# Performance work log

Measured on AMD Instinct MI355X. Metric: run time of the kernel, lower is better.

The kernel has to match this reference:

```python
import jax, jax.numpy as jnp
import numpy as np

D_K = 64  # per-head dim; source hardcodes d_k for the 1/sqrt(d_k) scale


def setup_inputs() -> dict:
    key = jax.random.key(0)
    kq, kk, kv = jax.random.split(key, 3)
    shape = (4, 16, 2048, D_K)  # [B, H, S, d]
    return {
        "q_s": jax.random.normal(kq, shape, dtype=jnp.float32),
        "k_s": jax.random.normal(kk, shape, dtype=jnp.float32),
        "v_s": jax.random.normal(kv, shape, dtype=jnp.float32),
    }


def reference(q_s, k_s, v_s):
    # scores = Q K^T / sqrt(d_k)  -> [B, H, S, S] (full matrix, unfused, as in source)
    scale = 1.0 / jnp.sqrt(jnp.asarray(D_K, dtype=q_s.dtype))
    scores = jnp.einsum("bhqd,bhkd->bhqk", q_s, k_s) * scale
    attn = jax.nn.softmax(scores, axis=-1)
    # out = attn @ V -> [B, H, S, d]
    return jnp.einsum("bhqk,bhkd->bhqd", attn, v_s)
```

## Files before the change

kernel.cpp:

```cpp
#include <hip/hip_runtime.h>
#include <stdint.h>
#include <math.h>

#define S_LEN 2048
#define DIM   64
#define QBLK  64
#define KVBLK 32
#define NKV   (S_LEN / KVBLK)

typedef __attribute__((ext_vector_type(8))) short short8;
typedef __attribute__((ext_vector_type(4))) float f32x4;

static __device__ __forceinline__ unsigned short f2bf(float f) {
    union { float f; uint32_t u; } cv; cv.f = f;
    uint32_t u = cv.u;
    return (unsigned short)((u + 0x7fffu + ((u >> 16) & 1u)) >> 16);
}

static __device__ __forceinline__ void gload16(const void* g, void* l) {
    __builtin_amdgcn_global_load_lds(
        (const __attribute__((address_space(1))) unsigned int*)g,
        (__attribute__((address_space(3))) unsigned int*)l, 16, 0, 0);
}

static __device__ __forceinline__ float vmax3(float a, float b, float c) {
    float d;
    asm("v_max3_f32 %0, %1, %2, %3" : "=v"(d) : "v"(a), "v"(b), "v"(c));
    return d;
}

__global__ void cvt_k(const float* __restrict__ kp, unsigned short* __restrict__ kws) {
    const int idx = blockIdx.x * 256 + threadIdx.x;
    const int c   = idx & 7;
    const int s   = (idx >> 3) & (S_LEN - 1);
    const int bh  = idx >> 14;
    const float* src = kp + ((size_t)bh * S_LEN + s) * DIM + c * 8;
    const f32x4 a = *reinterpret_cast<const f32x4*>(src);
    const f32x4 b = *reinterpret_cast<const f32x4*>(src + 4);
    short8 t;
    t[0] = (short)f2bf(a[0]); t[1] = (short)f2bf(a[1]);
    t[2] = (short)f2bf(a[2]); t[3] = (short)f2bf(a[3]);
    t[4] = (short)f2bf(b[0]); t[5] = (short)f2bf(b[1]);
    t[6] = (short)f2bf(b[2]); t[7] = (short)f2bf(b[3]);
    unsigned short* dst = kws + ((size_t)bh * S_LEN + s) * DIM + (size_t)((c ^ (s & 7)) * 8);
    *reinterpret_cast<short8*>(dst) = t;
}

__global__ void cvt_v(const float* __restrict__ vp, unsigned short* __restrict__ vtws) {
    const int bh = blockIdx.x >> 5;
    const int T  = blockIdx.x & 31;
    const int tid = threadIdx.x;
    __shared__ unsigned short ldsT[DIM][72];

    const int i = tid >> 2;
    const int dbase = (tid & 3) * 16;
    const float* src = vp + ((size_t)bh * S_LEN + T * 64 + i) * DIM + dbase;
#pragma unroll
    for (int q4 = 0; q4 < 4; ++q4) {
        const f32x4 a = *reinterpret_cast<const f32x4*>(src + q4 * 4);
#pragma unroll
        for (int j = 0; j < 4; ++j) ldsT[dbase + q4 * 4 + j][i] = f2bf(a[j]);
    }
    __syncthreads();
#pragma unroll
    for (int hh = 0; hh < 2; ++hh) {
        const int slot = tid + hh * 256;
        const int d = slot >> 3;
        const int h = (slot >> 2) & 1;
        const int c_st = slot & 3;
        const int cl = c_st ^ ((d >> 1) & 3);
        short8 t8;
#pragma unroll
        for (int j = 0; j < 8; ++j) {
            const int p = cl * 8 + j;
            const int kap = ((p & 4) << 2) | ((p & 16) >> 1) | ((p & 8) >> 1) | (p & 3);
            t8[j] = (short)ldsT[d][h * 32 + kap];
        }
        unsigned short* dst = vtws + ((size_t)bh * DIM + d) * S_LEN + T * 64 + h * 32 + c_st * 8;
        *reinterpret_cast<short8*>(dst) = t8;
    }
}

__global__ __launch_bounds__(256, 8)
void attn_fwd(const float* __restrict__ qp, const unsigned short* __restrict__ kws,
              const unsigned short* __restrict__ vtws, float* __restrict__ op) {
    const int lb = (blockIdx.x & 7) * 256 + (blockIdx.x >> 3);
    const int bh = lb >> 5;
    const int qb = lb & 31;
    const int tid  = threadIdx.x;
    const int wave = tid >> 6;
    const int lane = tid & 63;
    const int g = lane >> 4;
    const int r = lane & 15;

    __shared__ unsigned short klds[2][KVBLK * DIM];
    __shared__ unsigned short vlds[2][DIM * 32];

    const float*          qg    = qp   + (size_t)bh * (S_LEN * DIM);
    const unsigned short* kbase = kws  + (size_t)bh * (S_LEN * DIM);
    const unsigned short* vbase = vtws + (size_t)bh * (S_LEN * DIM);
    float*                og    = op   + (size_t)bh * (S_LEN * DIM);

    const float qscale = 0.125f * 1.44269504088896340736f;
    const int q0 = qb * QBLK + wave * 16;
    short8 qfrag[2];
    {
        const float* qrow = qg + (size_t)(q0 + r) * DIM;
#pragma unroll
        for (int ks = 0; ks < 2; ++ks) {
            const f32x4 a = *reinterpret_cast<const f32x4*>(qrow + ks * 32 + 8 * g);
            const f32x4 b = *reinterpret_cast<const f32x4*>(qrow + ks * 32 + 8 * g + 4);
            short8 t;
            t[0] = (short)f2bf(a[0] * qscale); t[1] = (short)f2bf(a[1] * qscale);
            t[2] = (short)f2bf(a[2] * qscale); t[3] = (short)f2bf(a[3] * qscale);
            t[4] = (short)f2bf(b[0] * qscale); t[5] = (short)f2bf(b[1] * qscale);
            t[6] = (short)f2bf(b[2] * qscale); t[7] = (short)f2bf(b[3] * qscale);
            qfrag[ks] = t;
        }
    }

    f32x4 o[4];
#pragma unroll
    for (int nt = 0; nt < 4; ++nt) { f32x4 z = {0.f, 0.f, 0.f, 0.f}; o[nt] = z; }
    float m_run = -INFINITY, l_part = 0.0f;

    const int srow = lane >> 3, schk = lane & 7;
    const int vd = wave * 16 + ((lane >> 2) & 15), vcst = lane & 3;
    auto stage = [&](int t, int buf) {
        gload16(kbase + (size_t)(t * KVBLK + wave * 8 + srow) * DIM + schk * 8,
                &klds[buf][(wave * 8) * DIM]);
        gload16(vbase + (size_t)vd * S_LEN + (t >> 1) * 64 + (t & 1) * 32 + vcst * 8,
                &vlds[buf][wave * 512]);
    };

    int koff[2][2], voff[4];
#pragma unroll
    for (int nt = 0; nt < 2; ++nt)
#pragma unroll
        for (int ks = 0; ks < 2; ++ks)
            koff[nt][ks] = (nt * 16 + r) * DIM + (((ks << 2) | g) ^ (r & 7)) * 8;
#pragma unroll
    for (int nt = 0; nt < 4; ++nt)
        voff[nt] = (nt * 16 + r) * 32 + (g ^ ((r >> 1) & 3)) * 8;

    const f32x4 z4 = {0.f, 0.f, 0.f, 0.f};

    stage(0, 0);
    __syncthreads();
    int cur = 0;

    for (int t = 0; t < NKV; ++t) {
        if (t + 1 < NKV) stage(t + 1, cur ^ 1);

        const unsigned short* kl = &klds[cur][0];
        __builtin_amdgcn_s_setprio(1);
        const short8 kf00 = *reinterpret_cast<const short8*>(kl + koff[0][0]);
        const short8 kf01 = *reinterpret_cast<const short8*>(kl + koff[0][1]);
        const short8 kf10 = *reinterpret_cast<const short8*>(kl + koff[1][0]);
        const short8 kf11 = *reinterpret_cast<const short8*>(kl + koff[1][1]);
        f32x4 st0 = __builtin_amdgcn_mfma_f32_16x16x32_bf16(kf00, qfrag[0], z4, 0, 0, 0);
        f32x4 st1 = __builtin_amdgcn_mfma_f32_16x16x32_bf16(kf10, qfrag[0], z4, 0, 0, 0);
        st0 = __builtin_amdgcn_mfma_f32_16x16x32_bf16(kf01, qfrag[1], st0, 0, 0, 0);
        st1 = __builtin_amdgcn_mfma_f32_16x16x32_bf16(kf11, qfrag[1], st1, 0, 0, 0);
        __builtin_amdgcn_s_setprio(0);

        const float a0 = vmax3(st0[0], st0[1], st0[2]);
        const float a1 = vmax3(st0[3], st1[0], st1[1]);
        const float a2 = fmaxf(st1[2], st1[3]);
        const float lane_mx = vmax3(a0, a1, a2);
        if (__any(lane_mx > m_run + 8.0f)) {
            float mx = fmaxf(lane_mx, __shfl_xor(lane_mx, 16));
            mx = fmaxf(mx, __shfl_xor(mx, 32));
            const float mnew = fmaxf(m_run, mx);
            const float al = __builtin_amdgcn_exp2f(m_run - mnew);
            m_run = mnew;
            l_part *= al;
#pragma unroll
            for (int nt = 0; nt < 4; ++nt) {
                f32x4 sc = o[nt];
                sc[0] *= al; sc[1] *= al; sc[2] *= al; sc[3] *= al;
                o[nt] = sc;
            }
        }
        f32x4 p0, p1;
        p0[0] = __builtin_amdgcn_exp2f(st0[0] - m_run);
        p0[1] = __builtin_amdgcn_exp2f(st0[1] - m_run);
        p0[2] = __builtin_amdgcn_exp2f(st0[2] - m_run);
        p0[3] = __builtin_amdgcn_exp2f(st0[3] - m_run);
        p1[0] = __builtin_amdgcn_exp2f(st1[0] - m_run);
        p1[1] = __builtin_amdgcn_exp2f(st1[1] - m_run);
        p1[2] = __builtin_amdgcn_exp2f(st1[2] - m_run);
        p1[3] = __builtin_amdgcn_exp2f(st1[3] - m_run);
        l_part += ((p0[0] + p0[1]) + (p0[2] + p0[3])) + ((p1[0] + p1[1]) + (p1[2] + p1[3]));

        short8 pfrag;
        {
            union { uint32_t u[4]; short8 v; } fr;
            asm("v_cvt_pk_bf16_f32 %0, %1, %2" : "=v"(fr.u[0]) : "v"(p0[0]), "v"(p0[1]));
            asm("v_cvt_pk_bf16_f32 %0, %1, %2" : "=v"(fr.u[1]) : "v"(p0[2]), "v"(p0[3]));
            asm("v_cvt_pk_bf16_f32 %0, %1, %2" : "=v"(fr.u[2]) : "v"(p1[0]), "v"(p1[1]));
            asm("v_cvt_pk_bf16_f32 %0, %1, %2" : "=v"(fr.u[3]) : "v"(p1[2]), "v"(p1[3]));
            pfrag = fr.v;
        }

        const unsigned short* vl = &vlds[cur][0];
        __builtin_amdgcn_s_setprio(1);
#pragma unroll
        for (int nt = 0; nt < 4; ++nt) {
            const short8 vf = *reinterpret_cast<const short8*>(vl + voff[nt]);
            o[nt] = __builtin_amdgcn_mfma_f32_16x16x32_bf16(vf, pfrag, o[nt], 0, 0, 0);
        }
        __builtin_amdgcn_s_setprio(0);

        __syncthreads();
        cur ^= 1;
    }

    float lfull = l_part;
    lfull += __shfl_xor(lfull, 16);
    lfull += __shfl_xor(lfull, 32);
    const float inv = 1.0f / lfull;
    float* dst = og + (size_t)(q0 + r) * DIM + 4 * g;
#pragma unroll
    for (int nt = 0; nt < 4; ++nt) {
        f32x4 tt = o[nt];
        tt[0] *= inv; tt[1] *= inv; tt[2] *= inv; tt[3] *= inv;
        *reinterpret_cast<f32x4*>(dst + nt * 16) = tt;
    }
}

extern "C" void kernel_launch(void* const* d_in, const int* in_sizes, int n_in,
                              void* d_out, int out_size, void* d_ws, size_t ws_size,
                              hipStream_t stream) {
    const float* q = (const float*)d_in[0];
    const float* k = (const float*)d_in[1];
    const float* v = (const float*)d_in[2];
    float* out = (float*)d_out;
    unsigned short* kws  = (unsigned short*)d_ws;
    unsigned short* vtws = kws + (size_t)64 * S_LEN * DIM;
    cvt_k<<<dim3(64 * S_LEN * 8 / 256), 256, 0, stream>>>(k, kws);
    cvt_v<<<dim3(64 * (S_LEN / 64)), 256, 0, stream>>>(v, vtws);
    attn_fwd<<<dim3(2048), 256, 0, stream>>>(q, kws, vtws, out);
}
```

Measured before the change: 121.3 us.

## Load K/V fragments directly from global memory instead of staging through LDS

Removes the double-buffered LDS staging of K and V tiles, along with the per-iteration block barrier. Each wave now reads its MFMA operand fragments straight from the pre-swizzled bf16 workspaces in global memory. The launch bound drops from 8 to 5 blocks per CU, which gives the compiler more registers to hold in-flight loads. The cost is that all four waves fetch the same K/V data redundantly through the cache hierarchy. There is also no explicit prefetch of the next tile, so load latency is exposed unless the compiler or occupancy hides it.

```diff
diff --git a/kernel.cpp b/kernel.cpp
--- a/kernel.cpp
+++ b/kernel.cpp
@@ -15,12 +15,6 @@
     union { float f; uint32_t u; } cv; cv.f = f;
     uint32_t u = cv.u;
     return (unsigned short)((u + 0x7fffu + ((u >> 16) & 1u)) >> 16);
-}
-
-static __device__ __forceinline__ void gload16(const void* g, void* l) {
-    __builtin_amdgcn_global_load_lds(
-        (const __attribute__((address_space(1))) unsigned int*)g,
-        (__attribute__((address_space(3))) unsigned int*)l, 16, 0, 0);
 }
 
 static __device__ __forceinline__ float vmax3(float a, float b, float c) {
@@ -81,7 +75,7 @@
     }
 }
 
-__global__ __launch_bounds__(256, 8)
+__global__ __launch_bounds__(256, 5)
 void attn_fwd(const float* __restrict__ qp, const unsigned short* __restrict__ kws,
               const unsigned short* __restrict__ vtws, float* __restrict__ op) {
     const int lb = (blockIdx.x & 7) * 256 + (blockIdx.x >> 3);
@@ -93,9 +87,6 @@
     const int g = lane >> 4;
     const int r = lane & 15;
 
-    __shared__ unsigned short klds[2][KVBLK * DIM];
-    __shared__ unsigned short vlds[2][DIM * 32];
-
     const float*          qg    = qp   + (size_t)bh * (S_LEN * DIM);
     const unsigned short* kbase = kws  + (size_t)bh * (S_LEN * DIM);
     const unsigned short* vbase = vtws + (size_t)bh * (S_LEN * DIM);
@@ -124,15 +115,6 @@
     for (int nt = 0; nt < 4; ++nt) { f32x4 z = {0.f, 0.f, 0.f, 0.f}; o[nt] = z; }
     float m_run = -INFINITY, l_part = 0.0f;
 
-    const int srow = lane >> 3, schk = lane & 7;
-    const int vd = wave * 16 + ((lane >> 2) & 15), vcst = lane & 3;
-    auto stage = [&](int t, int buf) {
-        gload16(kbase + (size_t)(t * KVBLK + wave * 8 + srow) * DIM + schk * 8,
-                &klds[buf][(wave * 8) * DIM]);
-        gload16(vbase + (size_t)vd * S_LEN + (t >> 1) * 64 + (t & 1) * 32 + vcst * 8,
-                &vlds[buf][wave * 512]);
-    };
-
     int koff[2][2], voff[4];
 #pragma unroll
     for (int nt = 0; nt < 2; ++nt)
@@ -141,28 +123,29 @@
             koff[nt][ks] = (nt * 16 + r) * DIM + (((ks << 2) | g) ^ (r & 7)) * 8;
 #pragma unroll
     for (int nt = 0; nt < 4; ++nt)
-        voff[nt] = (nt * 16 + r) * 32 + (g ^ ((r >> 1) & 3)) * 8;
+        voff[nt] = (nt * 16 + r) * S_LEN + (g ^ ((r >> 1) & 3)) * 8;
 
     const f32x4 z4 = {0.f, 0.f, 0.f, 0.f};
 
-    stage(0, 0);
-    __syncthreads();
-    int cur = 0;
-
     for (int t = 0; t < NKV; ++t) {
-        if (t + 1 < NKV) stage(t + 1, cur ^ 1);
-
-        const unsigned short* kl = &klds[cur][0];
+        const int kt = t * (KVBLK * DIM);
+        const int vt = t * KVBLK;
+
+        const short8 kf00 = *reinterpret_cast<const short8*>(kbase + kt + koff[0][0]);
+        const short8 kf01 = *reinterpret_cast<const short8*>(kbase + kt + koff[0][1]);
+        const short8 kf10 = *reinterpret_cast<const short8*>(kbase + kt + koff[1][0]);
+        const short8 kf11 = *reinterpret_cast<const short8*>(kbase + kt + koff[1][1]);
         __builtin_amdgcn_s_setprio(1);
-        const short8 kf00 = *reinterpret_cast<const short8*>(kl + koff[0][0]);
-        const short8 kf01 = *reinterpret_cast<const short8*>(kl + koff[0][1]);
-        const short8 kf10 = *reinterpret_cast<const short8*>(kl + koff[1][0]);
-        const short8 kf11 = *reinterpret_cast<const short8*>(kl + koff[1][1]);
         f32x4 st0 = __builtin_amdgcn_mfma_f32_16x16x32_bf16(kf00, qfrag[0], z4, 0, 0, 0);
         f32x4 st1 = __builtin_amdgcn_mfma_f32_16x16x32_bf16(kf10, qfrag[0], z4, 0, 0, 0);
         st0 = __builtin_amdgcn_mfma_f32_16x16x32_bf16(kf01, qfrag[1], st0, 0, 0, 0);
         st1 = __builtin_amdgcn_mfma_f32_16x16x32_bf16(kf11, qfrag[1], st1, 0, 0, 0);
         __builtin_amdgcn_s_setprio(0);
+
+        const short8 vf0 = *reinterpret_cast<const short8*>(vbase + vt + voff[0]);
+        const short8 vf1 = *reinterpret_cast<const short8*>(vbase + vt + voff[1]);
+        const short8 vf2 = *reinterpret_cast<const short8*>(vbase + vt + voff[2]);
+        const short8 vf3 = *reinterpret_cast<const short8*>(vbase + vt + voff[3]);
 
         const float a0 = vmax3(st0[0], st0[1], st0[2]);
         const float a1 = vmax3(st0[3], st1[0], st1[1]);
@@ -203,17 +186,12 @@
             pfrag = fr.v;
         }
 
-        const unsigned short* vl = &vlds[cur][0];
         __builtin_amdgcn_s_setprio(1);
-#pragma unroll
-        for (int nt = 0; nt < 4; ++nt) {
-            const short8 vf = *reinterpret_cast<const short8*>(vl + voff[nt]);
-            o[nt] = __builtin_amdgcn_mfma_f32_16x16x32_bf16(vf, pfrag, o[nt], 0, 0, 0);
-        }
+        o[0] = __builtin_amdgcn_mfma_f32_16x16x32_bf16(vf0, pfrag, o[0], 0, 0, 0);
+        o[1] = __builtin_amdgcn_mfma_f32_16x16x32_bf16(vf1, pfrag, o[1], 0, 0, 0);
+        o[2] = __builtin_amdgcn_mfma_f32_16x16x32_bf16(vf2, pfrag, o[2], 0, 0, 0);
+        o[3] = __builtin_amdgcn_mfma_f32_16x16x32_bf16(vf3, pfrag, o[3], 0, 0, 0);
         __builtin_amdgcn_s_setprio(0);
-
-        __syncthreads();
-        cur ^= 1;
     }
 
     float lfull = l_part;
```

Result: slower. 235.6 us (+94.3%).

## Double query tile per wave and software-pipeline QK with softmax-PV

Applied to the files above, without the earlier changes.

Each wave now handles 32 query rows (two 16-row tiles), so every K and V fragment read from LDS feeds twice as many MFMAs. The block count is halved and launch bounds drop to 4 blocks per CU. The main loop is restructured into a two-stage software pipeline: the QK^T scores for tile t+1 are computed while softmax and PV run for tile t, with K and V staging split and offset. This is meant to cut LDS traffic per FLOP and hide MFMA/exp latency, at the cost of more registers and lower occupancy.

```diff
diff --git a/kernel.cpp b/kernel.cpp
--- a/kernel.cpp
+++ b/kernel.cpp
@@ -4,7 +4,7 @@
 
 #define S_LEN 2048
 #define DIM   64
-#define QBLK  64
+#define QBLK  128
 #define KVBLK 32
 #define NKV   (S_LEN / KVBLK)
 
@@ -81,12 +81,78 @@
     }
 }
 
-__global__ __launch_bounds__(256, 8)
+#define QK_TILE(ST, KL)                                                                               \
+    do {                                                                                              \
+        __builtin_amdgcn_s_setprio(1);                                                                \
+        _Pragma("unroll")                                                                             \
+        for (int nt = 0; nt < 2; ++nt) {                                                              \
+            const short8 kf0 = *reinterpret_cast<const short8*>((KL) + koff[nt][0]);                  \
+            const short8 kf1 = *reinterpret_cast<const short8*>((KL) + koff[nt][1]);                  \
+            ST[0][nt] = __builtin_amdgcn_mfma_f32_16x16x32_bf16(kf0, qfrag[0][0], z4, 0, 0, 0);       \
+            ST[1][nt] = __builtin_amdgcn_mfma_f32_16x16x32_bf16(kf0, qfrag[1][0], z4, 0, 0, 0);       \
+            ST[0][nt] = __builtin_amdgcn_mfma_f32_16x16x32_bf16(kf1, qfrag[0][1], ST[0][nt], 0, 0, 0);\
+            ST[1][nt] = __builtin_amdgcn_mfma_f32_16x16x32_bf16(kf1, qfrag[1][1], ST[1][nt], 0, 0, 0);\
+        }                                                                                             \
+        __builtin_amdgcn_s_setprio(0);                                                                \
+    } while (0)
+
+#define SMPV(ST, VL)                                                                                  \
+    do {                                                                                              \
+        short8 pfA, pfB;                                                                              \
+        _Pragma("unroll")                                                                             \
+        for (int mt = 0; mt < 2; ++mt) {                                                              \
+            const f32x4 s0 = ST[mt][0], s1 = ST[mt][1];                                               \
+            const float a0 = vmax3(s0[0], s0[1], s0[2]);                                              \
+            const float a1 = vmax3(s0[3], s1[0], s1[1]);                                              \
+            const float lane_mx = vmax3(a0, a1, fmaxf(s1[2], s1[3]));                                 \
+            if (__any(lane_mx > m_run[mt] + 8.0f)) {                                                  \
+                float mx = fmaxf(lane_mx, __shfl_xor(lane_mx, 16));                                   \
+                mx = fmaxf(mx, __shfl_xor(mx, 32));                                                   \
+                const float mnew = fmaxf(m_run[mt], mx);                                              \
+                const float al = __builtin_amdgcn_exp2f(m_run[mt] - mnew);                            \
+                m_run[mt] = mnew;                                                                     \
+                l_part[mt] *= al;                                                                     \
+                _Pragma("unroll")                                                                     \
+                for (int nt = 0; nt < 4; ++nt) {                                                      \
+                    f32x4 sc = o[mt][nt];                                                             \
+                    sc[0] *= al; sc[1] *= al; sc[2] *= al; sc[3] *= al;                               \
+                    o[mt][nt] = sc;                                                                   \
+                }                                                                                     \
+            }                                                                                         \
+            const float mnow = m_run[mt];                                                             \
+            f32x4 p0, p1;                                                                             \
+            p0[0] = __builtin_amdgcn_exp2f(ST[mt][0][0] - mnow);                                      \
+            p0[1] = __builtin_amdgcn_exp2f(ST[mt][0][1] - mnow);                                      \
+            p0[2] = __builtin_amdgcn_exp2f(ST[mt][0][2] - mnow);                                      \
+            p0[3] = __builtin_amdgcn_exp2f(ST[mt][0][3] - mnow);                                      \
+            p1[0] = __builtin_amdgcn_exp2f(ST[mt][1][0] - mnow);                                      \
+            p1[1] = __builtin_amdgcn_exp2f(ST[mt][1][1] - mnow);                                      \
+            p1[2] = __builtin_amdgcn_exp2f(ST[mt][1][2] - mnow);                                      \
+            p1[3] = __builtin_amdgcn_exp2f(ST[mt][1][3] - mnow);                                      \
+            l_part[mt] += ((p0[0] + p0[1]) + (p0[2] + p0[3])) + ((p1[0] + p1[1]) + (p1[2] + p1[3])); \
+            union { uint32_t u[4]; short8 v; } fr;                                                    \
+            asm("v_cvt_pk_bf16_f32 %0, %1, %2" : "=v"(fr.u[0]) : "v"(p0[0]), "v"(p0[1]));             \
+            asm("v_cvt_pk_bf16_f32 %0, %1, %2" : "=v"(fr.u[1]) : "v"(p0[2]), "v"(p0[3]));             \
+            asm("v_cvt_pk_bf16_f32 %0, %1, %2" : "=v"(fr.u[2]) : "v"(p1[0]), "v"(p1[1]));             \
+            asm("v_cvt_pk_bf16_f32 %0, %1, %2" : "=v"(fr.u[3]) : "v"(p1[2]), "v"(p1[3]));             \
+            if (mt == 0) pfA = fr.v; else pfB = fr.v;                                                 \
+        }                                                                                             \
+        __builtin_amdgcn_s_setprio(1);                                                                \
+        _Pragma("unroll")                                                                             \
+        for (int ntd = 0; ntd < 4; ++ntd) {                                                           \
+            const short8 vf = *reinterpret_cast<const short8*>((VL) + voff[ntd]);                     \
+            o[0][ntd] = __builtin_amdgcn_mfma_f32_16x16x32_bf16(vf, pfA, o[0][ntd], 0, 0, 0);         \
+            o[1][ntd] = __builtin_amdgcn_mfma_f32_16x16x32_bf16(vf, pfB, o[1][ntd], 0, 0, 0);         \
+        }                                                                                             \
+        __builtin_amdgcn_s_setprio(0);                                                                \
+    } while (0)
+
+__global__ __launch_bounds__(256, 4)
 void attn_fwd(const float* __restrict__ qp, const unsigned short* __restrict__ kws,
               const unsigned short* __restrict__ vtws, float* __restrict__ op) {
-    const int lb = (blockIdx.x & 7) * 256 + (blockIdx.x >> 3);
-    const int bh = lb >> 5;
-    const int qb = lb & 31;
+    const int lb = (blockIdx.x & 7) * 128 + (blockIdx.x >> 3);
+    const int bh = lb >> 4;
+    const int qb = lb & 15;
     const int tid  = threadIdx.x;
     const int wave = tid >> 6;
     const int lane = tid & 63;
@@ -102,10 +168,11 @@
     float*                og    = op   + (size_t)bh * (S_LEN * DIM);
 
     const float qscale = 0.125f * 1.44269504088896340736f;
-    const int q0 = qb * QBLK + wave * 16;
-    short8 qfrag[2];
-    {
-        const float* qrow = qg + (size_t)(q0 + r) * DIM;
+    const int q0 = qb * QBLK + wave * 32;
+    short8 qfrag[2][2];
+#pragma unroll
+    for (int mt = 0; mt < 2; ++mt) {
+        const float* qrow = qg + (size_t)(q0 + mt * 16 + r) * DIM;
 #pragma unroll
         for (int ks = 0; ks < 2; ++ks) {
             const f32x4 a = *reinterpret_cast<const f32x4*>(qrow + ks * 32 + 8 * g);
@@ -115,20 +182,26 @@
             t[2] = (short)f2bf(a[2] * qscale); t[3] = (short)f2bf(a[3] * qscale);
             t[4] = (short)f2bf(b[0] * qscale); t[5] = (short)f2bf(b[1] * qscale);
             t[6] = (short)f2bf(b[2] * qscale); t[7] = (short)f2bf(b[3] * qscale);
-            qfrag[ks] = t;
+            qfrag[mt][ks] = t;
         }
     }
 
-    f32x4 o[4];
-#pragma unroll
-    for (int nt = 0; nt < 4; ++nt) { f32x4 z = {0.f, 0.f, 0.f, 0.f}; o[nt] = z; }
-    float m_run = -INFINITY, l_part = 0.0f;
+    f32x4 o[2][4];
+    float m_run[2], l_part[2];
+#pragma unroll
+    for (int mt = 0; mt < 2; ++mt) {
+#pragma unroll
+        for (int nt = 0; nt < 4; ++nt) { f32x4 z = {0.f, 0.f, 0.f, 0.f}; o[mt][nt] = z; }
+        m_run[mt] = -INFINITY; l_part[mt] = 0.0f;
+    }
 
     const int srow = lane >> 3, schk = lane & 7;
     const int vd = wave * 16 + ((lane >> 2) & 15), vcst = lane & 3;
-    auto stage = [&](int t, int buf) {
+    auto stageK = [&](int t, int buf) {
         gload16(kbase + (size_t)(t * KVBLK + wave * 8 + srow) * DIM + schk * 8,
                 &klds[buf][(wave * 8) * DIM]);
+    };
+    auto stageV = [&](int t, int buf) {
         gload16(vbase + (size_t)vd * S_LEN + (t >> 1) * 64 + (t & 1) * 32 + vcst * 8,
                 &vlds[buf][wave * 512]);
     };
@@ -144,88 +217,50 @@
         voff[nt] = (nt * 16 + r) * 32 + (g ^ ((r >> 1) & 3)) * 8;
 
     const f32x4 z4 = {0.f, 0.f, 0.f, 0.f};
-
-    stage(0, 0);
-    __syncthreads();
-    int cur = 0;
-
-    for (int t = 0; t < NKV; ++t) {
-        if (t + 1 < NKV) stage(t + 1, cur ^ 1);
-
-        const unsigned short* kl = &klds[cur][0];
-        __builtin_amdgcn_s_setprio(1);
-        const short8 kf00 = *reinterpret_cast<const short8*>(kl + koff[0][0]);
-        const short8 kf01 = *reinterpret_cast<const short8*>(kl + koff[0][1]);
-        const short8 kf10 = *reinterpret_cast<const short8*>(kl + koff[1][0]);
-        const short8 kf11 = *reinterpret_cast<const short8*>(kl + koff[1][1]);
-        f32x4 st0 = __builtin_amdgcn_mfma_f32_16x16x32_bf16(kf00, qfrag[0], z4, 0, 0, 0);
-        f32x4 st1 = __builtin_amdgcn_mfma_f32_16x16x32_bf16(kf10, qfrag[0], z4, 0, 0, 0);
-        st0 = __builtin_amdgcn_mfma_f32_16x16x32_bf16(kf01, qfrag[1], st0, 0, 0, 0);
-        st1 = __builtin_amdgcn_mfma_f32_16x16x32_bf16(kf11, qfrag[1], st1, 0, 0, 0);
-        __builtin_amdgcn_s_setprio(0);
-
-        const float a0 = vmax3(st0[0], st0[1], st0[2]);
-        const float a1 = vmax3(st0[3], st1[0], st1[1]);
-        const float a2 = fmaxf(st1[2], st1[3]);
-        const float lane_mx = vmax3(a0, a1, a2);
-        if (__any(lane_mx > m_run + 8.0f)) {
-            float mx = fmaxf(lane_mx, __shfl_xor(lane_mx, 16));
-            mx = fmaxf(mx, __shfl_xor(mx, 32));
-            const float mnew = fmaxf(m_run, mx);
-            const float al = __builtin_amdgcn_exp2f(m_run - mnew);
-            m_run = mnew;
-            l_part *= al;
-#pragma unroll
-            for (int nt = 0; nt < 4; ++nt) {
-                f32x4 sc = o[nt];
-                sc[0] *= al; sc[1] *= al; sc[2] *= al; sc[3] *= al;
-                o[nt] = sc;
-            }
+    const unsigned short* kl0 = &klds[0][0];
+    const unsigned short* kl1 = &klds[1][0];
+    const unsigned short* vl0 = &vlds[0][0];
+    const unsigned short* vl1 = &vlds[1][0];
+
+    f32x4 stA[2][2], stB[2][2];
+
+    stageK(0, 0);
+    __syncthreads();
+    stageK(1, 1); stageV(0, 0);
+    QK_TILE(stA, kl0);
+    __syncthreads();
+    stageK(2, 0); stageV(1, 1);
+    QK_TILE(stB, kl1);
+    SMPV(stA, vl0);
+    __syncthreads();
+
+    for (int tt = 2; tt < NKV; tt += 2) {
+        stageK(tt + 1, 1);
+        stageV(tt, 0);
+        QK_TILE(stA, kl0);
+        SMPV(stB, vl1);
+        __syncthreads();
+        if (tt + 2 < NKV) stageK(tt + 2, 0);
+        stageV(tt + 1, 1);
+        QK_TILE(stB, kl1);
+        SMPV(stA, vl0);
+        __syncthreads();
+    }
+    SMPV(stB, vl1);
+
+#pragma unroll
+    for (int mt = 0; mt < 2; ++mt) {
+        float lfull = l_part[mt];
+        lfull += __shfl_xor(lfull, 16);
+        lfull += __shfl_xor(lfull, 32);
+        const float inv = 1.0f / lfull;
+        float* dst = og + (size_t)(q0 + mt * 16 + r) * DIM + 4 * g;
+#pragma unroll
+        for (int ntd = 0; ntd < 4; ++ntd) {
+            f32x4 tt = o[mt][ntd];
+            tt[0] *= inv; tt[1] *= inv; tt[2] *= inv; tt[3] *= inv;
+            *reinterpret_cast<f32x4*>(dst + ntd * 16) = tt;
         }
-        f32x4 p0, p1;
-        p0[0] = __builtin_amdgcn_exp2f(st0[0] - m_run);
-        p0[1] = __builtin_amdgcn_exp2f(st0[1] - m_run);
-        p0[2] = __builtin_amdgcn_exp2f(st0[2] - m_run);
-        p0[3] = __builtin_amdgcn_exp2f(st0[3] - m_run);
-        p1[0] = __builtin_amdgcn_exp2f(st1[0] - m_run);
-        p1[1] = __builtin_amdgcn_exp2f(st1[1] - m_run);
-        p1[2] = __builtin_amdgcn_exp2f(st1[2] - m_run);
-        p1[3] = __builtin_amdgcn_exp2f(st1[3] - m_run);
-        l_part += ((p0[0] + p0[1]) + (p0[2] + p0[3])) + ((p1[0] + p1[1]) + (p1[2] + p1[3]));
-
-        short8 pfrag;
-        {
-            union { uint32_t u[4]; short8 v; } fr;
-            asm("v_cvt_pk_bf16_f32 %0, %1, %2" : "=v"(fr.u[0]) : "v"(p0[0]), "v"(p0[1]));
-            asm("v_cvt_pk_bf16_f32 %0, %1, %2" : "=v"(fr.u[1]) : "v"(p0[2]), "v"(p0[3]));
-            asm("v_cvt_pk_bf16_f32 %0, %1, %2" : "=v"(fr.u[2]) : "v"(p1[0]), "v"(p1[1]));
-            asm("v_cvt_pk_bf16_f32 %0, %1, %2" : "=v"(fr.u[3]) : "v"(p1[2]), "v"(p1[3]));
-            pfrag = fr.v;
-        }
-
-        const unsigned short* vl = &vlds[cur][0];
-        __builtin_amdgcn_s_setprio(1);
-#pragma unroll
-        for (int nt = 0; nt < 4; ++nt) {
-            const short8 vf = *reinterpret_cast<const short8*>(vl + voff[nt]);
-            o[nt] = __builtin_amdgcn_mfma_f32_16x16x32_bf16(vf, pfrag, o[nt], 0, 0, 0);
-        }
-        __builtin_amdgcn_s_setprio(0);
-
-        __syncthreads();
-        cur ^= 1;
-    }
-
-    float lfull = l_part;
-    lfull += __shfl_xor(lfull, 16);
-    lfull += __shfl_xor(lfull, 32);
-    const float inv = 1.0f / lfull;
-    float* dst = og + (size_t)(q0 + r) * DIM + 4 * g;
-#pragma unroll
-    for (int nt = 0; nt < 4; ++nt) {
-        f32x4 tt = o[nt];
-        tt[0] *= inv; tt[1] *= inv; tt[2] *= inv; tt[3] *= inv;
-        *reinterpret_cast<f32x4*>(dst + nt * 16) = tt;
     }
 }
 
@@ -240,5 +275,5 @@
     unsigned short* vtws = kws + (size_t)64 * S_LEN * DIM;
     cvt_k<<<dim3(64 * S_LEN * 8 / 256), 256, 0, stream>>>(k, kws);
     cvt_v<<<dim3(64 * (S_LEN / 64)), 256, 0, stream>>>(v, vtws);
-    attn_fwd<<<dim3(2048), 256, 0, stream>>>(q, kws, vtws, out);
-}
+    attn_fwd<<<dim3(1024), 256, 0, stream>>>(q, kws, vtws, out);
+}
```

After: 106.8 us. 11.9% less time.
